# Optimization experiments

Hardware: AMD Instinct MI355X
Metric: run time of the kernel (lower is better)

## Reference

```python
import jax, jax.numpy as jnp
import numpy as np

N, E, H, K = 2000, 512, 8, 32
DH = E // H  # 64
CLAMP = 10000.0
LN_EPS = 1e-5


def _layernorm(x, g, b):
    mu = jnp.mean(x, axis=-1, keepdims=True)
    var = jnp.mean((x - mu) ** 2, axis=-1, keepdims=True)
    return (x - mu) * jax.lax.rsqrt(var + LN_EPS) * g + b


def setup_inputs() -> dict:
    key = jax.random.key(0)
    ks = jax.random.split(key, 16)
    s_in = 1.0 / np.sqrt(E)
    inp = {
        'x': jax.random.normal(ks[0], (N, E), jnp.float32),
        'coords9': jax.random.normal(ks[1], (N, 9), jnp.float32),
        'prompt_signal': jax.random.normal(ks[2], (E,), jnp.float32),
        # pos_encoder: Linear(3, E//4) + GELU + LayerNorm(E//4)
        'pos_w1': jax.random.normal(ks[3], (E // 4, 3), jnp.float32) * 0.5,
        'pos_b1': jax.random.normal(ks[4], (E // 4,), jnp.float32) * 0.02,
        'pos_ln_g': jnp.ones((E // 4,), jnp.float32),
        'pos_ln_b': jnp.zeros((E // 4,), jnp.float32),
        # MultiheadAttention in/out projections
        'wq': jax.random.normal(ks[5], (E, E), jnp.float32) * s_in,
        'wk': jax.random.normal(ks[6], (E, E), jnp.float32) * s_in,
        'wv': jax.random.normal(ks[7], (E, E), jnp.float32) * s_in,
        'bq': jnp.zeros((E,), jnp.float32),
        'bk': jnp.zeros((E,), jnp.float32),
        'bv': jnp.zeros((E,), jnp.float32),
        'wo': jax.random.normal(ks[8], (E, E), jnp.float32) * s_in,
        'bo': jnp.zeros((E,), jnp.float32),
    }
    return inp


def reference(x, coords9, prompt_signal, pos_w1, pos_b1, pos_ln_g, pos_ln_b,
              wq, wk, wv, bq, bk, bv, wo, bo):
    n = x.shape[0]
    # centroids of triangle faces: (N,3)
    centroids = coords9.reshape(n, 3, 3).mean(axis=1)
    # pairwise centroid distances (only relation feature that affects output)
    diff = centroids[:, None, :] - centroids[None, :, :]        # (N,N,3)
    distances = jnp.linalg.norm(diff, axis=-1)                   # (N,N)
    # positional encoding branch
    pos_enc = _layernorm(jax.nn.gelu(centroids @ pos_w1.T + pos_b1, approximate=False),
                         pos_ln_g, pos_ln_b)                     # (N,E/4)
    prompt_enhanced = x + prompt_signal[None, :]
    pos_enhanced = jnp.concatenate([prompt_enhanced[:, :3 * E // 4], pos_enc], axis=-1)  # (N,E)
    # top-k nearest neighbors mask (k smallest distances per row)
    _, topk_idx = jax.lax.top_k(-distances, K)                   # (N,K)
    attn_mask = jnp.full((n, n), -jnp.inf, jnp.float32)
    attn_mask = attn_mask.at[jnp.arange(n)[:, None], topk_idx].set(0.0)
    # multi-head attention, self q=k=v, fp32
    q = (pos_enhanced @ wq.T + bq).reshape(n, H, DH)
    k = (pos_enhanced @ wk.T + bk).reshape(n, H, DH)
    v = (pos_enhanced @ wv.T + bv).reshape(n, H, DH)
    scores = jnp.einsum('nhd,mhd->hnm', q, k) / np.sqrt(DH) + attn_mask[None]
    attn = jax.nn.softmax(scores, axis=-1)                       # (H,N,N)
    ctx = jnp.einsum('hnm,mhd->nhd', attn, v).reshape(n, E)
    out = ctx @ wo.T + bo
    # _sanitize_tensor
    out = jnp.nan_to_num(out, nan=0.0, posinf=CLAMP, neginf=-CLAMP)
    return jnp.clip(out, -CLAMP, CLAMP)
```

## Files before the change

kernel.cpp:

```cpp
#include <hip/hip_runtime.h>
#include <math.h>

#define NN_K 32
#define E_DIM 512
#define CLAMP_V 10000.0f

typedef __attribute__((ext_vector_type(8))) short short8;
typedef __attribute__((ext_vector_type(4))) float f32x4;

__device__ __forceinline__ unsigned short f2bf(float x) {
  unsigned u = __float_as_uint(x);
  unsigned r = u + 0x7fffu + ((u >> 16) & 1u);
  return (unsigned short)(r >> 16);
}
__device__ __forceinline__ float bf2f_bits(short h) {
  return __uint_as_float(((unsigned)(unsigned short)h) << 16);
}

__device__ __forceinline__ void async16(const void* g, void* l) {
  __builtin_amdgcn_global_load_lds((const __attribute__((address_space(1))) void*)g,
                                   (__attribute__((address_space(3))) void*)l, 16, 0, 0);
}

__global__ __launch_bounds__(256) void front_kernel(
    const float* __restrict__ x, const float* __restrict__ coords9,
    const float* __restrict__ prompt,
    const float* __restrict__ w1, const float* __restrict__ b1,
    const float* __restrict__ ln_g, const float* __restrict__ ln_b,
    const float* __restrict__ wq, const float* __restrict__ wk,
    const float* __restrict__ wv, const float* __restrict__ wo,
    short* __restrict__ w_bf, short* __restrict__ pos_bf,
    int* __restrict__ topk, int N, int Mpad)
{
  int blk = blockIdx.x;
  int t = threadIdx.x;

  if (blk < 256) {
    #pragma unroll
    for (int i = 0; i < 4; ++i) {
      int v = blk * 256 + t + i * 65536;
      int m = v >> 16;
      int e = v & 0xffff;
      const float* src = m == 0 ? wq : (m == 1 ? wk : (m == 2 ? wv : wo));
      float4 f = ((const float4*)src)[e];
      short4 h;
      h.x = (short)f2bf(f.x); h.y = (short)f2bf(f.y);
      h.z = (short)f2bf(f.z); h.w = (short)f2bf(f.w);
      ((short4*)w_bf)[v] = h;
    }
    return;
  }

  if (blk < 2304) {
    int n = blk - 256;
    size_t rb = (size_t)n * E_DIM;
    if (n >= N) {
      #pragma unroll
      for (int j = t; j < E_DIM; j += 256) pos_bf[rb + j] = 0;
      return;
    }
    __shared__ float red[4];
    float g = 0.f;
    if (t < 128) {
      const float* c9 = coords9 + n * 9;
      float c0 = (c9[0] + c9[3] + c9[6]) / 3.0f;
      float c1 = (c9[1] + c9[4] + c9[7]) / 3.0f;
      float c2 = (c9[2] + c9[5] + c9[8]) / 3.0f;
      float pre = c0 * w1[t*3+0] + c1 * w1[t*3+1] + c2 * w1[t*3+2] + b1[t];
      g = 0.5f * pre * (1.0f + erff(pre * 0.70710678118654752440f));
      float s = g;
      #pragma unroll
      for (int o = 32; o > 0; o >>= 1) s += __shfl_xor(s, o);
      if ((t & 63) == 0) red[t >> 6] = s;
    }
    __syncthreads();
    float mu = (red[0] + red[1]) * (1.0f / 128.0f);
    float d = g - mu;
    if (t < 128) {
      float s2 = d * d;
      #pragma unroll
      for (int o = 32; o > 0; o >>= 1) s2 += __shfl_xor(s2, o);
      if ((t & 63) == 0) red[2 + (t >> 6)] = s2;
    }
    __syncthreads();
    if (t < 128) {
      float var = (red[2] + red[3]) * (1.0f / 128.0f);
      float y = d * rsqrtf(var + 1e-5f) * ln_g[t] + ln_b[t];
      pos_bf[rb + 384 + t] = (short)f2bf(y);
    }
    #pragma unroll
    for (int j = t; j < 384; j += 256)
      pos_bf[rb + j] = (short)f2bf(x[rb + j] + prompt[j]);
    return;
  }

  {
    __shared__ unsigned hist[256];
    __shared__ unsigned waveSums[4];
    __shared__ unsigned sel_bin, sel_rem;
    __shared__ unsigned cnt, tcnt;
    __shared__ unsigned tie[2048];

    int n = blk - 2304;
    int lane = t & 63, wid = t >> 6;
    const float* cn = coords9 + n * 9;
    float cx = (cn[0] + cn[3] + cn[6]) / 3.0f;
    float cy = (cn[1] + cn[4] + cn[7]) / 3.0f;
    float cz = (cn[2] + cn[5] + cn[8]) / 3.0f;

    unsigned bits[8];
    #pragma unroll
    for (int r = 0; r < 8; ++r) {
      int m = t + (r << 8);
      unsigned b = 0xFFFFFFFFu;
      if (m < N) {
        const float* cm = coords9 + m * 9;
        float mx_ = (cm[0] + cm[3] + cm[6]) / 3.0f;
        float my_ = (cm[1] + cm[4] + cm[7]) / 3.0f;
        float mz_ = (cm[2] + cm[5] + cm[8]) / 3.0f;
        float dx = cx - mx_, dy = cy - my_, dz = cz - mz_;
        float dist = sqrtf(dx*dx + dy*dy + dz*dz);
        b = __float_as_uint(dist);
      }
      bits[r] = b;
    }

    unsigned prefix = 0;
    unsigned K_rem = NN_K;
    #pragma unroll
    for (int p = 0; p < 4; ++p) {
      int shift = 24 - 8 * p;
      unsigned high_mask = (p == 0) ? 0u : (0xFFFFFFFFu << (8 * (4 - p)));
      hist[t] = 0;
      __syncthreads();
      #pragma unroll
      for (int r = 0; r < 8; ++r) {
        if ((bits[r] & high_mask) == prefix)
          atomicAdd(&hist[(bits[r] >> shift) & 255], 1u);
      }
      __syncthreads();
      unsigned h = hist[t];
      unsigned scan = h;
      #pragma unroll
      for (int o = 1; o < 64; o <<= 1) {
        unsigned u = __shfl_up(scan, o);
        if (lane >= o) scan += u;
      }
      if (lane == 63) waveSums[wid] = scan;
      __syncthreads();
      unsigned off = 0;
      for (int w = 0; w < wid; ++w) off += waveSums[w];
      scan += off;
      if (scan >= K_rem && (scan - h) < K_rem) {
        sel_bin = (unsigned)t;
        sel_rem = K_rem - (scan - h);
      }
      __syncthreads();
      prefix |= sel_bin << shift;
      K_rem = sel_rem;
      __syncthreads();
    }

    unsigned T = prefix;
    if (t == 0) { cnt = 0; tcnt = 0; }
    __syncthreads();
    #pragma unroll
    for (int r = 0; r < 8; ++r) {
      int m = t + (r << 8);
      if (m < N) {
        if (bits[r] < T) {
          unsigned slot = atomicAdd(&cnt, 1u);
          topk[n * NN_K + slot] = m;
        } else if (bits[r] == T) {
          unsigned tp = atomicAdd(&tcnt, 1u);
          tie[tp] = (unsigned)m;
        }
      }
    }
    __syncthreads();
    if (t == 0) {
      unsigned base = cnt;
      unsigned need = K_rem;
      for (unsigned it = 0; it < need; ++it) {
        unsigned best = 0xFFFFFFFFu, bj = 0;
        for (unsigned j = 0; j < tcnt; ++j)
          if (tie[j] < best) { best = tie[j]; bj = j; }
        topk[n * NN_K + base + it] = (int)best;
        tie[bj] = 0xFFFFFFFFu;
      }
    }
  }
}

__device__ __forceinline__ void gemm_core(
    const short* __restrict__ A, const short* __restrict__ W,
    const float* __restrict__ bias,
    float* __restrict__ outf, short* __restrict__ outb,
    int out_ld, int out_c0,
    int M, int row0, int col0, bool doClamp)
{
  __shared__ short sA[2][64 * 32], sB[2][128 * 32];
  int tid = threadIdx.x;
  int cr = tid >> 2;
  int ck = (tid & 3) << 3;
  const short* gA = A + (size_t)(row0 + cr) * 512 + ck;
  const short* gB = W + (size_t)(col0 + cr) * 512 + ck;
  int lo = tid * 8, loB1 = (tid + 256) * 8;
  const size_t rstep = (size_t)64 * 512;

  int lane = tid & 63, wv_ = tid >> 6;
  int wn = wv_ << 5;
  int lr = lane & 15, lq = lane >> 4;

#define STAGE(t, b) do { \
    async16(gA + (t) * 32,         &sA[b][lo]); \
    async16(gB + (t) * 32,         &sB[b][lo]); \
    async16(gB + (t) * 32 + rstep, &sB[b][loB1]); } while (0)

  STAGE(0, 0);
  STAGE(1, 1);

  f32x4 acc[4][2];
  #pragma unroll
  for (int i = 0; i < 4; ++i)
    #pragma unroll
    for (int j = 0; j < 2; ++j)
      acc[i][j] = (f32x4){0.f, 0.f, 0.f, 0.f};

  #pragma unroll
  for (int it = 0; it < 16; ++it) {
    int cur = it & 1;
    if (it == 15) asm volatile("s_waitcnt vmcnt(0)\ns_barrier" ::: "memory");
    else          asm volatile("s_waitcnt vmcnt(3)\ns_barrier" ::: "memory");

    short8 af[4], bf[2];
    #pragma unroll
    for (int i = 0; i < 4; ++i)
      af[i] = *(const short8*)&sA[cur][((i << 4) + lr) * 32 + (lq << 3)];
    #pragma unroll
    for (int j = 0; j < 2; ++j)
      bf[j] = *(const short8*)&sB[cur][(wn + (j << 4) + lr) * 32 + (lq << 3)];
    #pragma unroll
    for (int i = 0; i < 4; ++i)
      #pragma unroll
      for (int j = 0; j < 2; ++j)
        acc[i][j] = __builtin_amdgcn_mfma_f32_16x16x32_bf16(af[i], bf[j], acc[i][j], 0, 0, 0);

    asm volatile("s_waitcnt lgkmcnt(0)\ns_barrier" ::: "memory");
    if (it + 2 < 16) STAGE(it + 2, cur);
  }
#undef STAGE

  #pragma unroll
  for (int j = 0; j < 2; ++j) {
    int gcol = col0 + wn + (j << 4) + lr;
    float bv_ = bias[gcol];
    #pragma unroll
    for (int i = 0; i < 4; ++i) {
      #pragma unroll
      for (int r = 0; r < 4; ++r) {
        int grow = row0 + (i << 4) + (lq << 2) + r;
        if (grow < M) {
          float v = acc[i][j][r] + bv_;
          if (doClamp) {
            v = isnan(v) ? 0.0f : v;
            v = fminf(fmaxf(v, -CLAMP_V), CLAMP_V);
          }
          if (outf) outf[(size_t)grow * 512 + gcol] = v;
          else      outb[(size_t)grow * out_ld + out_c0 + gcol] = (short)f2bf(v);
        }
      }
    }
  }
}

__global__ __launch_bounds__(256) void qkv_mfma(
    const short* __restrict__ A, const short* __restrict__ Wb,
    const float* __restrict__ bq, const float* __restrict__ bk, const float* __restrict__ bv,
    float* __restrict__ qb, short* __restrict__ kv, int M)
{
  int sel = blockIdx.y >> 2;
  int nblk = blockIdx.y & 3;
  int r0 = blockIdx.x * 64, c0 = nblk * 128;
  if (sel == 0)
    gemm_core(A, Wb, bq, qb, nullptr, 512, 0, M, r0, c0, false);
  else if (sel == 1)
    gemm_core(A, Wb + 262144, bk, nullptr, kv, 1024, 0, M, r0, c0, false);
  else
    gemm_core(A, Wb + 2 * 262144, bv, nullptr, kv, 1024, 512, M, r0, c0, false);
}

__global__ __launch_bounds__(256) void out_mfma(
    const short* __restrict__ A, const short* __restrict__ Wb,
    const float* __restrict__ bias, float* __restrict__ out, int M)
{
  gemm_core(A, Wb + (size_t)3 * 262144, bias, out, nullptr, 512, 0, M,
            blockIdx.x * 64, blockIdx.y * 128, true);
}

__global__ __launch_bounds__(512) void attn_kernel(
    const float* __restrict__ qb, const short* __restrict__ kv,
    const int* __restrict__ topk, short* __restrict__ ctx_bf, int N)
{
  __shared__ short klds[32 * 512];
  __shared__ int sidx[NN_K];
  __shared__ float plds[8 * 32];

  int n = blockIdx.x;
  int tid = threadIdx.x;
  size_t rb = (size_t)n * E_DIM;
  if (n >= N) { ctx_bf[rb + tid] = 0; return; }

  if (tid < NN_K) sidx[tid] = topk[n * NN_K + tid];
  __syncthreads();

  int h = tid >> 6, lane = tid & 63;
  int jk = lane & 31, half = lane >> 5;
  int dbase = h * 64 + half * 32;

  float qv[32];
  {
    const float4* qs = (const float4*)(qb + rb + dbase);
    #pragma unroll
    for (int b = 0; b < 8; ++b) {
      float4 f = qs[b];
      qv[b*4+0] = f.x; qv[b*4+1] = f.y; qv[b*4+2] = f.z; qv[b*4+3] = f.w;
    }
  }

  {
    int j = tid >> 4, a = tid & 15;
    const short8* src = (const short8*)(kv + (size_t)sidx[j] * 1024 + a * 32);
    int sw = 4 * (j & 15);
    short* row = &klds[j * 512];
    #pragma unroll
    for (int b = 0; b < 4; ++b) {
      short8 val = src[b];
      int d0 = a * 32 + b * 8;
      *(short4*)&row[(d0    ) ^ sw] = *(const short4*)&val;
      *(short4*)&row[(d0 + 4) ^ sw] = *((const short4*)&val + 1);
    }
  }
  __syncthreads();

  float s = 0.f;
  {
    int sw = 4 * (jk & 15);
    const short* krow = &klds[jk * 512];
    #pragma unroll
    for (int i4 = 0; i4 < 8; ++i4) {
      short4 kkv = *(const short4*)&krow[(dbase + i4 * 4) ^ sw];
      s += qv[i4*4+0] * bf2f_bits(kkv.x) + qv[i4*4+1] * bf2f_bits(kkv.y)
         + qv[i4*4+2] * bf2f_bits(kkv.z) + qv[i4*4+3] * bf2f_bits(kkv.w);
    }
  }
  s += __shfl_xor(s, 32);
  s *= 0.125f;

  float mx = s;
  #pragma unroll
  for (int o = 16; o > 0; o >>= 1) mx = fmaxf(mx, __shfl_xor(mx, o));
  float p = expf(s - mx);
  float l = p;
  #pragma unroll
  for (int o = 16; o > 0; o >>= 1) l += __shfl_xor(l, o);
  p *= (1.0f / l);
  if (half == 0) plds[h * 32 + jk] = p;
  __syncthreads();

  float pv[32];
  #pragma unroll
  for (int b = 0; b < 8; ++b) {
    float4 f = *(const float4*)&plds[h * 32 + b * 4];
    pv[b*4+0] = f.x; pv[b*4+1] = f.y; pv[b*4+2] = f.z; pv[b*4+3] = f.w;
  }

  int off = 512 + h * 64 + lane;
  float acc = 0.f;
  #pragma unroll
  for (int j = 0; j < NN_K; ++j)
    acc += pv[j] * bf2f_bits(kv[(size_t)sidx[j] * 1024 + off]);
  ctx_bf[rb + h * 64 + lane] = (short)f2bf(acc);
}

extern "C" void kernel_launch(void* const* d_in, const int* in_sizes, int n_in,
                              void* d_out, int out_size, void* d_ws, size_t ws_size,
                              hipStream_t stream) {
  const float* x       = (const float*)d_in[0];
  const float* coords9 = (const float*)d_in[1];
  const float* prompt  = (const float*)d_in[2];
  const float* pos_w1  = (const float*)d_in[3];
  const float* pos_b1  = (const float*)d_in[4];
  const float* ln_g    = (const float*)d_in[5];
  const float* ln_b    = (const float*)d_in[6];
  const float* wq      = (const float*)d_in[7];
  const float* wk      = (const float*)d_in[8];
  const float* wv      = (const float*)d_in[9];
  const float* bq      = (const float*)d_in[10];
  const float* bk      = (const float*)d_in[11];
  const float* bv      = (const float*)d_in[12];
  const float* wo      = (const float*)d_in[13];
  const float* bo      = (const float*)d_in[14];

  int N = in_sizes[1] / 9;
  int Mpad = (N + 127) & ~127;
  size_t PE = (size_t)Mpad * E_DIM;

  char* p = (char*)d_ws;
  short* pos_bf = (short*)p; p += PE * 2;
  short* w_bf   = (short*)p; p += (size_t)4 * 512 * 512 * 2;
  float* qb     = (float*)p; p += PE * 4;
  short* kv_bf  = (short*)p; p += PE * 2 * 2;
  short* ctx_bf = (short*)p; p += PE * 2;
  int*   topk   = (int*)p;

  front_kernel<<<256 + Mpad + N, 256, 0, stream>>>(
      x, coords9, prompt, pos_w1, pos_b1, ln_g, ln_b,
      wq, wk, wv, wo, w_bf, pos_bf, topk, N, Mpad);

  dim3 gq(Mpad / 64, 12);
  qkv_mfma<<<gq, 256, 0, stream>>>(pos_bf, w_bf, bq, bk, bv, qb, kv_bf, Mpad);
  attn_kernel<<<Mpad, 512, 0, stream>>>(qb, kv_bf, topk, ctx_bf, N);

  dim3 go(Mpad / 64, 4);
  out_mfma<<<go, 256, 0, stream>>>(ctx_bf, w_bf, bo, (float*)d_out, N);
}
```

Baseline: 152.9 us.

## Fuse all four kernels into one persistent mega-kernel with grid barriers

Replaces the four separate launches (front prep, QKV GEMM, attention, output GEMM) with a single persistent kernel of 768 blocks that synchronises phases through atomic-counter grid barriers. GEMM tiles shrink to 64x64 so each phase maps onto the fixed grid, and attention runs 256 threads handling two heads per wave. The aim is to remove launch and inter-kernel gaps. The cost is spin-wait barrier overhead, a hard requirement that all 768 blocks be co-resident (deadlock risk otherwise), and smaller, less efficient GEMM tiles.

Result: slower. 430.5 us (+181.6%).

```diff
diff --git a/kernel.cpp b/kernel.cpp
--- a/kernel.cpp
+++ b/kernel.cpp
@@ -4,6 +4,7 @@
 #define NN_K 32
 #define E_DIM 512
 #define CLAMP_V 10000.0f
+#define NBLK 768
 
 typedef __attribute__((ext_vector_type(8))) short short8;
 typedef __attribute__((ext_vector_type(4))) float f32x4;
@@ -16,31 +17,126 @@
 __device__ __forceinline__ float bf2f_bits(short h) {
   return __uint_as_float(((unsigned)(unsigned short)h) << 16);
 }
-
 __device__ __forceinline__ void async16(const void* g, void* l) {
   __builtin_amdgcn_global_load_lds((const __attribute__((address_space(1))) void*)g,
                                    (__attribute__((address_space(3))) void*)l, 16, 0, 0);
 }
 
-__global__ __launch_bounds__(256) void front_kernel(
+__device__ __forceinline__ void grid_barrier(unsigned* cnt) {
+  __syncthreads();
+  if (threadIdx.x == 0) {
+    __threadfence();
+    atomicAdd(cnt, 1u);
+    while (atomicAdd(cnt, 0u) < NBLK) __builtin_amdgcn_s_sleep(2);
+    __threadfence();
+  }
+  __syncthreads();
+}
+
+__device__ __forceinline__ void gemm64(
+    const short* __restrict__ A, const short* __restrict__ W,
+    const float* __restrict__ bias,
+    float* __restrict__ outf, short* __restrict__ outb,
+    int out_ld, int out_c0, int Mstore, int row0, int col0, bool doClamp,
+    short (*sA)[2048], short (*sB)[2048])
+{
+  int t = threadIdx.x;
+  int cr = t >> 2, ck = (t & 3) << 3;
+  const short* gA = A + (size_t)(row0 + cr) * 512 + ck;
+  const short* gB = W + (size_t)(col0 + cr) * 512 + ck;
+  int lo = t * 8;
+  int lane = t & 63, w = t >> 6;
+  int wm = (w & 1) << 5, wn = (w >> 1) << 5;
+  int lr = lane & 15, lq = lane >> 4;
+
+#define STG(tt, b) { async16(gA + (tt) * 32, &sA[b][lo]); \
+                     async16(gB + (tt) * 32, &sB[b][lo]); }
+  STG(0, 0);
+  STG(1, 1);
+
+  f32x4 acc[2][2];
+  #pragma unroll
+  for (int i = 0; i < 2; ++i)
+    #pragma unroll
+    for (int j = 0; j < 2; ++j)
+      acc[i][j] = (f32x4){0.f, 0.f, 0.f, 0.f};
+
+  #pragma unroll
+  for (int it = 0; it < 16; ++it) {
+    int cur = it & 1;
+    if (it == 15) asm volatile("s_waitcnt vmcnt(0)\ns_barrier" ::: "memory");
+    else          asm volatile("s_waitcnt vmcnt(2)\ns_barrier" ::: "memory");
+
+    short8 af[2], bfr[2];
+    #pragma unroll
+    for (int i = 0; i < 2; ++i) {
+      af[i]  = *(const short8*)&sA[cur][(wm + (i << 4) + lr) * 32 + (lq << 3)];
+      bfr[i] = *(const short8*)&sB[cur][(wn + (i << 4) + lr) * 32 + (lq << 3)];
+    }
+    #pragma unroll
+    for (int i = 0; i < 2; ++i)
+      #pragma unroll
+      for (int j = 0; j < 2; ++j)
+        acc[i][j] = __builtin_amdgcn_mfma_f32_16x16x32_bf16(af[i], bfr[j], acc[i][j], 0, 0, 0);
+
+    asm volatile("s_waitcnt lgkmcnt(0)\ns_barrier" ::: "memory");
+    if (it + 2 < 16) STG(it + 2, cur);
+  }
+#undef STG
+
+  #pragma unroll
+  for (int j = 0; j < 2; ++j) {
+    int gcol = col0 + wn + (j << 4) + lr;
+    float bv_ = bias[gcol];
+    #pragma unroll
+    for (int i = 0; i < 2; ++i) {
+      #pragma unroll
+      for (int rr = 0; rr < 4; ++rr) {
+        int grow = row0 + wm + (i << 4) + (lq << 2) + rr;
+        if (grow < Mstore) {
+          float v = acc[i][j][rr] + bv_;
+          if (doClamp) {
+            v = isnan(v) ? 0.0f : v;
+            v = fminf(fmaxf(v, -CLAMP_V), CLAMP_V);
+          }
+          if (outf) outf[(size_t)grow * 512 + gcol] = v;
+          else      outb[(size_t)grow * out_ld + out_c0 + gcol] = (short)f2bf(v);
+        }
+      }
+    }
+  }
+}
+
+__global__ __launch_bounds__(256, 3) void mega_kernel(
     const float* __restrict__ x, const float* __restrict__ coords9,
     const float* __restrict__ prompt,
     const float* __restrict__ w1, const float* __restrict__ b1,
     const float* __restrict__ ln_g, const float* __restrict__ ln_b,
     const float* __restrict__ wq, const float* __restrict__ wk,
     const float* __restrict__ wv, const float* __restrict__ wo,
+    const float* __restrict__ bq, const float* __restrict__ bk,
+    const float* __restrict__ bv, const float* __restrict__ bo,
     short* __restrict__ w_bf, short* __restrict__ pos_bf,
-    int* __restrict__ topk, int N, int Mpad)
+    int* __restrict__ topkb, float* __restrict__ qb, short* __restrict__ kv,
+    short* __restrict__ ctx_bf, float* __restrict__ outp,
+    unsigned* __restrict__ bar, int N, int Mpad)
 {
-  int blk = blockIdx.x;
-  int t = threadIdx.x;
-
-  if (blk < 256) {
-    #pragma unroll
-    for (int i = 0; i < 4; ++i) {
-      int v = blk * 256 + t + i * 65536;
-      int m = v >> 16;
-      int e = v & 0xffff;
+  __shared__ union {
+    struct { float red[8]; } pos;
+    struct { unsigned hist[256]; unsigned waveSums[4];
+             unsigned sel_bin, sel_rem, cnt, tcnt; unsigned tie[2048]; } tk;
+    struct { short sA[2][2048]; short sB[2][2048]; } gm;
+    struct { short klds[16384]; int sidx[NN_K]; float plds[256]; } at;
+  } S;
+
+  int blk = blockIdx.x, t = threadIdx.x;
+  int lane = t & 63, wv_ = t >> 6;
+
+  #pragma unroll
+  for (int i = 0; i < 2; ++i) {
+    int v = blk * 256 + t + i * (NBLK * 256);
+    if (v < 262144) {
+      int m = v >> 16, e = v & 0xffff;
       const float* src = m == 0 ? wq : (m == 1 ? wk : (m == 2 ? wv : wo));
       float4 f = ((const float4*)src)[e];
       short4 h;
@@ -48,19 +144,17 @@
       h.z = (short)f2bf(f.z); h.w = (short)f2bf(f.w);
       ((short4*)w_bf)[v] = h;
     }
-    return;
-  }
-
-  if (blk < 2304) {
-    int n = blk - 256;
+  }
+  for (int r = 0; r < 3; ++r) {
+    int n = blk + r * NBLK;
+    if (n >= Mpad) break;
     size_t rb = (size_t)n * E_DIM;
     if (n >= N) {
-      #pragma unroll
       for (int j = t; j < E_DIM; j += 256) pos_bf[rb + j] = 0;
-      return;
-    }
-    __shared__ float red[4];
-    float g = 0.f;
+      continue;
+    }
+    __syncthreads();
+    float g = 0.f, d = 0.f;
     if (t < 128) {
       const float* c9 = coords9 + n * 9;
       float c0 = (c9[0] + c9[3] + c9[6]) / 3.0f;
@@ -71,47 +165,38 @@
       float s = g;
       #pragma unroll
       for (int o = 32; o > 0; o >>= 1) s += __shfl_xor(s, o);
-      if ((t & 63) == 0) red[t >> 6] = s;
-    }
-    __syncthreads();
-    float mu = (red[0] + red[1]) * (1.0f / 128.0f);
-    float d = g - mu;
+      if ((t & 63) == 0) S.pos.red[t >> 6] = s;
+    }
+    __syncthreads();
     if (t < 128) {
+      float mu = (S.pos.red[0] + S.pos.red[1]) * (1.0f / 128.0f);
+      d = g - mu;
       float s2 = d * d;
       #pragma unroll
       for (int o = 32; o > 0; o >>= 1) s2 += __shfl_xor(s2, o);
-      if ((t & 63) == 0) red[2 + (t >> 6)] = s2;
+      if ((t & 63) == 0) S.pos.red[2 + (t >> 6)] = s2;
     }
     __syncthreads();
     if (t < 128) {
-      float var = (red[2] + red[3]) * (1.0f / 128.0f);
+      float var = (S.pos.red[2] + S.pos.red[3]) * (1.0f / 128.0f);
       float y = d * rsqrtf(var + 1e-5f) * ln_g[t] + ln_b[t];
       pos_bf[rb + 384 + t] = (short)f2bf(y);
     }
-    #pragma unroll
     for (int j = t; j < 384; j += 256)
       pos_bf[rb + j] = (short)f2bf(x[rb + j] + prompt[j]);
-    return;
-  }
-
-  {
-    __shared__ unsigned hist[256];
-    __shared__ unsigned waveSums[4];
-    __shared__ unsigned sel_bin, sel_rem;
-    __shared__ unsigned cnt, tcnt;
-    __shared__ unsigned tie[2048];
-
-    int n = blk - 2304;
-    int lane = t & 63, wid = t >> 6;
+  }
+  for (int r = 0; r < 3; ++r) {
+    int n = blk + r * NBLK;
+    if (n >= N) break;
+    __syncthreads();
     const float* cn = coords9 + n * 9;
     float cx = (cn[0] + cn[3] + cn[6]) / 3.0f;
     float cy = (cn[1] + cn[4] + cn[7]) / 3.0f;
     float cz = (cn[2] + cn[5] + cn[8]) / 3.0f;
-
     unsigned bits[8];
     #pragma unroll
-    for (int r = 0; r < 8; ++r) {
-      int m = t + (r << 8);
+    for (int rr = 0; rr < 8; ++rr) {
+      int m = t + (rr << 8);
       unsigned b = 0xFFFFFFFFu;
       if (m < N) {
         const float* cm = coords9 + m * 9;
@@ -119,268 +204,171 @@
         float my_ = (cm[1] + cm[4] + cm[7]) / 3.0f;
         float mz_ = (cm[2] + cm[5] + cm[8]) / 3.0f;
         float dx = cx - mx_, dy = cy - my_, dz = cz - mz_;
-        float dist = sqrtf(dx*dx + dy*dy + dz*dz);
-        b = __float_as_uint(dist);
-      }
-      bits[r] = b;
-    }
-
-    unsigned prefix = 0;
-    unsigned K_rem = NN_K;
+        b = __float_as_uint(sqrtf(dx*dx + dy*dy + dz*dz));
+      }
+      bits[rr] = b;
+    }
+    unsigned prefix = 0, K_rem = NN_K;
     #pragma unroll
     for (int p = 0; p < 4; ++p) {
       int shift = 24 - 8 * p;
       unsigned high_mask = (p == 0) ? 0u : (0xFFFFFFFFu << (8 * (4 - p)));
-      hist[t] = 0;
+      S.tk.hist[t] = 0;
       __syncthreads();
       #pragma unroll
-      for (int r = 0; r < 8; ++r) {
-        if ((bits[r] & high_mask) == prefix)
-          atomicAdd(&hist[(bits[r] >> shift) & 255], 1u);
-      }
+      for (int rr = 0; rr < 8; ++rr)
+        if ((bits[rr] & high_mask) == prefix)
+          atomicAdd(&S.tk.hist[(bits[rr] >> shift) & 255], 1u);
       __syncthreads();
-      unsigned h = hist[t];
+      unsigned h = S.tk.hist[t];
       unsigned scan = h;
       #pragma unroll
       for (int o = 1; o < 64; o <<= 1) {
         unsigned u = __shfl_up(scan, o);
         if (lane >= o) scan += u;
       }
-      if (lane == 63) waveSums[wid] = scan;
+      if (lane == 63) S.tk.waveSums[wv_] = scan;
       __syncthreads();
       unsigned off = 0;
-      for (int w = 0; w < wid; ++w) off += waveSums[w];
+      for (int w2 = 0; w2 < wv_; ++w2) off += S.tk.waveSums[w2];
       scan += off;
       if (scan >= K_rem && (scan - h) < K_rem) {
-        sel_bin = (unsigned)t;
-        sel_rem = K_rem - (scan - h);
+        S.tk.sel_bin = (unsigned)t;
+        S.tk.sel_rem = K_rem - (scan - h);
       }
       __syncthreads();
-      prefix |= sel_bin << shift;
-      K_rem = sel_rem;
+      prefix |= S.tk.sel_bin << shift;
+      K_rem = S.tk.sel_rem;
       __syncthreads();
     }
-
     unsigned T = prefix;
-    if (t == 0) { cnt = 0; tcnt = 0; }
-    __syncthreads();
-    #pragma unroll
-    for (int r = 0; r < 8; ++r) {
-      int m = t + (r << 8);
+    if (t == 0) { S.tk.cnt = 0; S.tk.tcnt = 0; }
+    __syncthreads();
+    #pragma unroll
+    for (int rr = 0; rr < 8; ++rr) {
+      int m = t + (rr << 8);
       if (m < N) {
-        if (bits[r] < T) {
-          unsigned slot = atomicAdd(&cnt, 1u);
-          topk[n * NN_K + slot] = m;
-        } else if (bits[r] == T) {
-          unsigned tp = atomicAdd(&tcnt, 1u);
-          tie[tp] = (unsigned)m;
+        if (bits[rr] < T) {
+          unsigned slot = atomicAdd(&S.tk.cnt, 1u);
+          topkb[n * NN_K + slot] = m;
+        } else if (bits[rr] == T) {
+          unsigned tp = atomicAdd(&S.tk.tcnt, 1u);
+          S.tk.tie[tp] = (unsigned)m;
         }
       }
     }
     __syncthreads();
     if (t == 0) {
-      unsigned base = cnt;
-      unsigned need = K_rem;
+      unsigned base = S.tk.cnt, need = K_rem;
       for (unsigned it = 0; it < need; ++it) {
         unsigned best = 0xFFFFFFFFu, bj = 0;
-        for (unsigned j = 0; j < tcnt; ++j)
-          if (tie[j] < best) { best = tie[j]; bj = j; }
-        topk[n * NN_K + base + it] = (int)best;
-        tie[bj] = 0xFFFFFFFFu;
-      }
-    }
-  }
-}
-
-__device__ __forceinline__ void gemm_core(
-    const short* __restrict__ A, const short* __restrict__ W,
-    const float* __restrict__ bias,
-    float* __restrict__ outf, short* __restrict__ outb,
-    int out_ld, int out_c0,
-    int M, int row0, int col0, bool doClamp)
-{
-  __shared__ short sA[2][64 * 32], sB[2][128 * 32];
-  int tid = threadIdx.x;
-  int cr = tid >> 2;
-  int ck = (tid & 3) << 3;
-  const short* gA = A + (size_t)(row0 + cr) * 512 + ck;
-  const short* gB = W + (size_t)(col0 + cr) * 512 + ck;
-  int lo = tid * 8, loB1 = (tid + 256) * 8;
-  const size_t rstep = (size_t)64 * 512;
-
-  int lane = tid & 63, wv_ = tid >> 6;
-  int wn = wv_ << 5;
-  int lr = lane & 15, lq = lane >> 4;
-
-#define STAGE(t, b) do { \
-    async16(gA + (t) * 32,         &sA[b][lo]); \
-    async16(gB + (t) * 32,         &sB[b][lo]); \
-    async16(gB + (t) * 32 + rstep, &sB[b][loB1]); } while (0)
-
-  STAGE(0, 0);
-  STAGE(1, 1);
-
-  f32x4 acc[4][2];
-  #pragma unroll
-  for (int i = 0; i < 4; ++i)
-    #pragma unroll
-    for (int j = 0; j < 2; ++j)
-      acc[i][j] = (f32x4){0.f, 0.f, 0.f, 0.f};
-
-  #pragma unroll
-  for (int it = 0; it < 16; ++it) {
-    int cur = it & 1;
-    if (it == 15) asm volatile("s_waitcnt vmcnt(0)\ns_barrier" ::: "memory");
-    else          asm volatile("s_waitcnt vmcnt(3)\ns_barrier" ::: "memory");
-
-    short8 af[4], bf[2];
-    #pragma unroll
-    for (int i = 0; i < 4; ++i)
-      af[i] = *(const short8*)&sA[cur][((i << 4) + lr) * 32 + (lq << 3)];
-    #pragma unroll
-    for (int j = 0; j < 2; ++j)
-      bf[j] = *(const short8*)&sB[cur][(wn + (j << 4) + lr) * 32 + (lq << 3)];
-    #pragma unroll
-    for (int i = 0; i < 4; ++i)
-      #pragma unroll
-      for (int j = 0; j < 2; ++j)
-        acc[i][j] = __builtin_amdgcn_mfma_f32_16x16x32_bf16(af[i], bf[j], acc[i][j], 0, 0, 0);
-
-    asm volatile("s_waitcnt lgkmcnt(0)\ns_barrier" ::: "memory");
-    if (it + 2 < 16) STAGE(it + 2, cur);
-  }
-#undef STAGE
-
-  #pragma unroll
-  for (int j = 0; j < 2; ++j) {
-    int gcol = col0 + wn + (j << 4) + lr;
-    float bv_ = bias[gcol];
-    #pragma unroll
-    for (int i = 0; i < 4; ++i) {
-      #pragma unroll
-      for (int r = 0; r < 4; ++r) {
-        int grow = row0 + (i << 4) + (lq << 2) + r;
-        if (grow < M) {
-          float v = acc[i][j][r] + bv_;
-          if (doClamp) {
-            v = isnan(v) ? 0.0f : v;
-            v = fminf(fmaxf(v, -CLAMP_V), CLAMP_V);
-          }
-          if (outf) outf[(size_t)grow * 512 + gcol] = v;
-          else      outb[(size_t)grow * out_ld + out_c0 + gcol] = (short)f2bf(v);
+        for (unsigned j = 0; j < S.tk.tcnt; ++j)
+          if (S.tk.tie[j] < best) { best = S.tk.tie[j]; bj = j; }
+        topkb[n * NN_K + base + it] = (int)best;
+        S.tk.tie[bj] = 0xFFFFFFFFu;
+      }
+    }
+  }
+
+  grid_barrier(&bar[0]);
+  {
+    int sel = blk / 256, rem = blk & 255;
+    int r0 = (rem >> 3) << 6, c0 = (rem & 7) << 6;
+    const short* W = w_bf + (size_t)sel * 262144;
+    if (sel == 0)
+      gemm64(pos_bf, W, bq, qb, nullptr, 512, 0, Mpad, r0, c0, false, S.gm.sA, S.gm.sB);
+    else if (sel == 1)
+      gemm64(pos_bf, W, bk, nullptr, kv, 1024, 0, Mpad, r0, c0, false, S.gm.sA, S.gm.sB);
+    else
+      gemm64(pos_bf, W, bv, nullptr, kv, 1024, 512, Mpad, r0, c0, false, S.gm.sA, S.gm.sB);
+  }
+
+  grid_barrier(&bar[1]);
+  for (int r = 0; r < 3; ++r) {
+    int n = blk + r * NBLK;
+    if (n >= Mpad) break;
+    size_t rb = (size_t)n * E_DIM;
+    __syncthreads();
+    if (n >= N) {
+      for (int j = t; j < E_DIM; j += 256) ctx_bf[rb + j] = 0;
+      continue;
+    }
+    if (t < NN_K) S.at.sidx[t] = topkb[n * NN_K + t];
+    {
+      int j = t >> 3, a = t & 7;
+      int row = topkb[n * NN_K + j];
+      const short8* src = (const short8*)(kv + (size_t)row * 1024 + a * 64);
+      int sw = 4 * (j & 15);
+      short* rowp = &S.at.klds[j * 512];
+      #pragma unroll
+      for (int b = 0; b < 8; ++b) {
+        short8 val = src[b];
+        int d0 = a * 64 + b * 8;
+        *(short4*)&rowp[(d0    ) ^ sw] = *(const short4*)&val;
+        *(short4*)&rowp[(d0 + 4) ^ sw] = *((const short4*)&val + 1);
+      }
+    }
+    __syncthreads();
+
+    int jk = lane & 31, half = lane >> 5;
+    #pragma unroll
+    for (int hp = 0; hp < 2; ++hp) {
+      int h = wv_ + hp * 4;
+      int dbase = h * 64 + half * 32;
+      float qv[32];
+      {
+        const float4* qs = (const float4*)(qb + rb + dbase);
+        #pragma unroll
+        for (int b = 0; b < 8; ++b) {
+          float4 f = qs[b];
+          qv[b*4+0] = f.x; qv[b*4+1] = f.y; qv[b*4+2] = f.z; qv[b*4+3] = f.w;
         }
       }
-    }
-  }
-}
-
-__global__ __launch_bounds__(256) void qkv_mfma(
-    const short* __restrict__ A, const short* __restrict__ Wb,
-    const float* __restrict__ bq, const float* __restrict__ bk, const float* __restrict__ bv,
-    float* __restrict__ qb, short* __restrict__ kv, int M)
-{
-  int sel = blockIdx.y >> 2;
-  int nblk = blockIdx.y & 3;
-  int r0 = blockIdx.x * 64, c0 = nblk * 128;
-  if (sel == 0)
-    gemm_core(A, Wb, bq, qb, nullptr, 512, 0, M, r0, c0, false);
-  else if (sel == 1)
-    gemm_core(A, Wb + 262144, bk, nullptr, kv, 1024, 0, M, r0, c0, false);
-  else
-    gemm_core(A, Wb + 2 * 262144, bv, nullptr, kv, 1024, 512, M, r0, c0, false);
-}
-
-__global__ __launch_bounds__(256) void out_mfma(
-    const short* __restrict__ A, const short* __restrict__ Wb,
-    const float* __restrict__ bias, float* __restrict__ out, int M)
-{
-  gemm_core(A, Wb + (size_t)3 * 262144, bias, out, nullptr, 512, 0, M,
-            blockIdx.x * 64, blockIdx.y * 128, true);
-}
-
-__global__ __launch_bounds__(512) void attn_kernel(
-    const float* __restrict__ qb, const short* __restrict__ kv,
-    const int* __restrict__ topk, short* __restrict__ ctx_bf, int N)
-{
-  __shared__ short klds[32 * 512];
-  __shared__ int sidx[NN_K];
-  __shared__ float plds[8 * 32];
-
-  int n = blockIdx.x;
-  int tid = threadIdx.x;
-  size_t rb = (size_t)n * E_DIM;
-  if (n >= N) { ctx_bf[rb + tid] = 0; return; }
-
-  if (tid < NN_K) sidx[tid] = topk[n * NN_K + tid];
-  __syncthreads();
-
-  int h = tid >> 6, lane = tid & 63;
-  int jk = lane & 31, half = lane >> 5;
-  int dbase = h * 64 + half * 32;
-
-  float qv[32];
-  {
-    const float4* qs = (const float4*)(qb + rb + dbase);
-    #pragma unroll
-    for (int b = 0; b < 8; ++b) {
-      float4 f = qs[b];
-      qv[b*4+0] = f.x; qv[b*4+1] = f.y; qv[b*4+2] = f.z; qv[b*4+3] = f.w;
-    }
-  }
-
-  {
-    int j = tid >> 4, a = tid & 15;
-    const short8* src = (const short8*)(kv + (size_t)sidx[j] * 1024 + a * 32);
-    int sw = 4 * (j & 15);
-    short* row = &klds[j * 512];
-    #pragma unroll
-    for (int b = 0; b < 4; ++b) {
-      short8 val = src[b];
-      int d0 = a * 32 + b * 8;
-      *(short4*)&row[(d0    ) ^ sw] = *(const short4*)&val;
-      *(short4*)&row[(d0 + 4) ^ sw] = *((const short4*)&val + 1);
-    }
-  }
-  __syncthreads();
-
-  float s = 0.f;
-  {
-    int sw = 4 * (jk & 15);
-    const short* krow = &klds[jk * 512];
-    #pragma unroll
-    for (int i4 = 0; i4 < 8; ++i4) {
-      short4 kkv = *(const short4*)&krow[(dbase + i4 * 4) ^ sw];
-      s += qv[i4*4+0] * bf2f_bits(kkv.x) + qv[i4*4+1] * bf2f_bits(kkv.y)
-         + qv[i4*4+2] * bf2f_bits(kkv.z) + qv[i4*4+3] * bf2f_bits(kkv.w);
-    }
-  }
-  s += __shfl_xor(s, 32);
-  s *= 0.125f;
-
-  float mx = s;
-  #pragma unroll
-  for (int o = 16; o > 0; o >>= 1) mx = fmaxf(mx, __shfl_xor(mx, o));
-  float p = expf(s - mx);
-  float l = p;
-  #pragma unroll
-  for (int o = 16; o > 0; o >>= 1) l += __shfl_xor(l, o);
-  p *= (1.0f / l);
-  if (half == 0) plds[h * 32 + jk] = p;
-  __syncthreads();
-
-  float pv[32];
-  #pragma unroll
-  for (int b = 0; b < 8; ++b) {
-    float4 f = *(const float4*)&plds[h * 32 + b * 4];
-    pv[b*4+0] = f.x; pv[b*4+1] = f.y; pv[b*4+2] = f.z; pv[b*4+3] = f.w;
-  }
-
-  int off = 512 + h * 64 + lane;
-  float acc = 0.f;
-  #pragma unroll
-  for (int j = 0; j < NN_K; ++j)
-    acc += pv[j] * bf2f_bits(kv[(size_t)sidx[j] * 1024 + off]);
-  ctx_bf[rb + h * 64 + lane] = (short)f2bf(acc);
+      float s = 0.f;
+      int sw = 4 * (jk & 15);
+      const short* krow = &S.at.klds[jk * 512];
+      #pragma unroll
+      for (int i4 = 0; i4 < 8; ++i4) {
+        short4 kk = *(const short4*)&krow[(dbase + i4 * 4) ^ sw];
+        s += qv[i4*4+0] * bf2f_bits(kk.x) + qv[i4*4+1] * bf2f_bits(kk.y)
+           + qv[i4*4+2] * bf2f_bits(kk.z) + qv[i4*4+3] * bf2f_bits(kk.w);
+      }
+      s += __shfl_xor(s, 32);
+      s *= 0.125f;
+      float mx = s;
+      #pragma unroll
+      for (int o = 16; o > 0; o >>= 1) mx = fmaxf(mx, __shfl_xor(mx, o));
+      float pp = expf(s - mx);
+      float l = pp;
+      #pragma unroll
+      for (int o = 16; o > 0; o >>= 1) l += __shfl_xor(l, o);
+      pp *= (1.0f / l);
+      if (half == 0) S.at.plds[h * 32 + jk] = pp;
+    }
+    #pragma unroll
+    for (int hp = 0; hp < 2; ++hp) {
+      int h = wv_ + hp * 4;
+      float pv[32];
+      #pragma unroll
+      for (int b = 0; b < 8; ++b) {
+        float4 f = *(const float4*)&S.at.plds[h * 32 + b * 4];
+        pv[b*4+0] = f.x; pv[b*4+1] = f.y; pv[b*4+2] = f.z; pv[b*4+3] = f.w;
+      }
+      int off = 512 + h * 64 + lane;
+      float acc = 0.f;
+      #pragma unroll
+      for (int j = 0; j < NN_K; ++j)
+        acc += pv[j] * bf2f_bits(kv[(size_t)S.at.sidx[j] * 1024 + off]);
+      ctx_bf[rb + h * 64 + lane] = (short)f2bf(acc);
+    }
+  }
+
+  grid_barrier(&bar[2]);
+  if (blk < 256) {
+    int r0 = (blk >> 3) << 6, c0 = (blk & 7) << 6;
+    gemm64(ctx_bf, w_bf + (size_t)3 * 262144, bo, outp, nullptr, 512, 0,
+           N, r0, c0, true, S.gm.sA, S.gm.sB);
+  }
 }
 
 extern "C" void kernel_launch(void* const* d_in, const int* in_sizes, int n_in,
@@ -412,16 +400,14 @@
   float* qb     = (float*)p; p += PE * 4;
   short* kv_bf  = (short*)p; p += PE * 2 * 2;
   short* ctx_bf = (short*)p; p += PE * 2;
-  int*   topk   = (int*)p;
-
-  front_kernel<<<256 + Mpad + N, 256, 0, stream>>>(
+  int*   topkb  = (int*)p;   p += (size_t)N * NN_K * 4;
+  p = (char*)(((uintptr_t)p + 255) & ~(uintptr_t)255);
+  unsigned* bar = (unsigned*)p;
+
+  hipMemsetAsync(bar, 0, 64, stream);
+  mega_kernel<<<NBLK, 256, 0, stream>>>(
       x, coords9, prompt, pos_w1, pos_b1, ln_g, ln_b,
-      wq, wk, wv, wo, w_bf, pos_bf, topk, N, Mpad);
-
-  dim3 gq(Mpad / 64, 12);
-  qkv_mfma<<<gq, 256, 0, stream>>>(pos_bf, w_bf, bq, bk, bv, qb, kv_bf, Mpad);
-  attn_kernel<<<Mpad, 512, 0, stream>>>(qb, kv_bf, topk, ctx_bf, N);
-
-  dim3 go(Mpad / 64, 4);
-  out_mfma<<<go, 256, 0, stream>>>(ctx_bf, w_bf, bo, (float*)d_out, N);
-}
+      wq, wk, wv, wo, bq, bk, bv, bo,
+      w_bf, pos_bf, topkb, qb, kv_bf, ctx_bf, (float*)d_out,
+      bar, N, Mpad);
+}
```
